# Optimization experiments

Hardware: AMD Instinct MI355X
Metric: run time of the kernel (lower is better)

The kernel has to match this reference:

```python
import jax, jax.numpy as jnp
import numpy as np

L, D, H, DK, DFF = 6, 768, 12, 64, 3072
VOCAB, NUM_BUCKETS, MAX_DIST = 32128, 32, 128
B, S = 8, 512
NEG = -1e9


def t5_layer_norm(x, w, eps=1e-6):
    var = jnp.mean(jnp.square(x), axis=-1, keepdims=True)
    return w * x * jax.lax.rsqrt(var + eps)


def relative_position_bucket(rel, num_buckets=NUM_BUCKETS, max_distance=MAX_DIST):
    # bidirectional T5 bucketing
    nb = num_buckets // 2
    ret = (rel > 0).astype(jnp.int32) * nb
    n = jnp.abs(rel)
    max_exact = nb // 2
    is_small = n < max_exact
    logf = jnp.log(jnp.maximum(n, 1).astype(jnp.float32) / max_exact)
    val_large = max_exact + (logf / np.log(max_distance / max_exact) * (nb - max_exact)).astype(jnp.int32)
    val_large = jnp.minimum(val_large, nb - 1)
    return ret + jnp.where(is_small, n, val_large)


def setup_inputs() -> dict:
    key = jax.random.key(0)
    ks = jax.random.split(key, 9)
    w = 0.02  # weight scale for numeric stability over 6 blocks
    return {
        "input_ids": jax.random.randint(ks[0], (B, S), 0, VOCAB),
        "attention_mask": jnp.ones((B, S), jnp.float32),
        "embed_w": jax.random.normal(ks[1], (VOCAB, D), jnp.float32),
        "ln1_w": jnp.ones((L, D), jnp.float32),
        "q_w": jax.random.normal(ks[2], (L, H * DK, D), jnp.float32) * w,
        "k_w": jax.random.normal(ks[3], (L, H * DK, D), jnp.float32) * w,
        "v_w": jax.random.normal(ks[4], (L, H * DK, D), jnp.float32) * w,
        "rel_bias_w": jax.random.normal(ks[5], (NUM_BUCKETS, H), jnp.float32),
        "o_w": jax.random.normal(ks[6], (L, D, H * DK), jnp.float32) * w,
        "ln2_w": jnp.ones((L, D), jnp.float32),
        "wi_w": jax.random.normal(ks[7], (L, DFF, D), jnp.float32) * w,
        "wo_w": jax.random.normal(ks[8], (L, D, DFF), jnp.float32) * w,
        "final_ln_w": jnp.ones((D,), jnp.float32),
    }


def reference(input_ids, attention_mask, embed_w, ln1_w, q_w, k_w, v_w,
              rel_bias_w, o_w, ln2_w, wi_w, wo_w, final_ln_w):
    b, s = input_ids.shape
    h = embed_w[input_ids]  # [B,S,D]

    # position bias computed once (block 0 owns the table; shared by all blocks)
    pos = jnp.arange(s)
    rel = pos[None, :] - pos[:, None]  # memory - query, [S,S]
    bucket = relative_position_bucket(rel)
    pos_bias = rel_bias_w[bucket]  # [S,S,H]
    pos_bias = jnp.transpose(pos_bias, (2, 0, 1))[None]  # [1,H,S,S]
    ext_mask = (1.0 - attention_mask)[:, None, None, :] * NEG  # [B,1,1,S]
    bias = pos_bias + ext_mask  # [B,H,S,S]

    for l in range(L):
        # --- self-attention (T5: no 1/sqrt(d) scaling) ---
        x = t5_layer_norm(h, ln1_w[l])
        q = jnp.einsum('bsd,id->bsi', x, q_w[l]).reshape(b, s, H, DK).transpose(0, 2, 1, 3)
        k = jnp.einsum('bsd,id->bsi', x, k_w[l]).reshape(b, s, H, DK).transpose(0, 2, 1, 3)
        v = jnp.einsum('bsd,id->bsi', x, v_w[l]).reshape(b, s, H, DK).transpose(0, 2, 1, 3)
        scores = jnp.einsum('bhqd,bhkd->bhqk', q, k) + bias
        attn = jax.nn.softmax(scores, axis=-1)
        ctx = jnp.einsum('bhqk,bhkd->bhqd', attn, v)
        ctx = ctx.transpose(0, 2, 1, 3).reshape(b, s, H * DK)
        h = h + jnp.einsum('bsi,di->bsd', ctx, o_w[l])
        # --- ReLU FFN ---
        x = t5_layer_norm(h, ln2_w[l])
        ff = jax.nn.relu(jnp.einsum('bsd,fd->bsf', x, wi_w[l]))
        h = h + jnp.einsum('bsf,df->bsd', ff, wo_w[l])

    return t5_layer_norm(h, final_ln_w)
```

## Files before the change

kernel.cpp:

```cpp
#include <hip/hip_runtime.h>
#include <hip/hip_bf16.h>
#include <math.h>

#define L_ 6
#define D_ 768
#define H_ 12
#define DK_ 64
#define DFF_ 3072
#define NB_ 32
#define MAXDIST_ 128
#define B_ 8
#define S_ 512
#define NEG_ (-1e9f)
#define BS_ (B_*S_)
#define BSD_ ((size_t)BS_*D_)
#define WLAYER_ 7077888

typedef __bf16 bf16x8 __attribute__((ext_vector_type(8)));
typedef float f32x4 __attribute__((ext_vector_type(4)));

__device__ __forceinline__ unsigned short f2bf(float f) {
    unsigned u = __float_as_uint(f);
    u += 0x7fff + ((u >> 16) & 1);
    return (unsigned short)(u >> 16);
}
__device__ __forceinline__ float bf2f(unsigned short s) {
    return __uint_as_float(((unsigned)s) << 16);
}

#define GLDS(g, l) __builtin_amdgcn_global_load_lds( \
    (const __attribute__((address_space(1))) void*)(const void*)(g), \
    (__attribute__((address_space(3))) void*)(void*)(l), 16, 0, 0)

__global__ __launch_bounds__(192) void k_embed(const int* __restrict__ ids,
                                               const float* __restrict__ ew,
                                               float* __restrict__ h) {
    int row = blockIdx.x;
    int id = ids[row];
    const float4* src = (const float4*)(ew + (size_t)id * D_);
    float4* dst = (float4*)(h + (size_t)row * D_);
    dst[threadIdx.x] = src[threadIdx.x];
}

template<int OUTBF>
__global__ __launch_bounds__(256) void k_rmsnorm(const float* __restrict__ in,
                                                 const float* __restrict__ w,
                                                 void* __restrict__ outp) {
    int row = blockIdx.x;
    int tid = threadIdx.x;
    const float* x = in + (size_t)row * D_;
    float ss = 0.f;
    for (int i = tid; i < D_; i += 256) { float v = x[i]; ss += v * v; }
    #pragma unroll
    for (int off = 32; off; off >>= 1) ss += __shfl_down(ss, off, 64);
    __shared__ float sbuf[4];
    if ((tid & 63) == 0) sbuf[tid >> 6] = ss;
    __syncthreads();
    float tot = sbuf[0] + sbuf[1] + sbuf[2] + sbuf[3];
    float scale = rsqrtf(tot / (float)D_ + 1e-6f);
    if (OUTBF) {
        unsigned short* o = (unsigned short*)outp + (size_t)row * D_;
        for (int i = tid; i < D_; i += 256) o[i] = f2bf(w[i] * x[i] * scale);
    } else {
        float* o = (float*)outp + (size_t)row * D_;
        for (int i = tid; i < D_; i += 256) o[i] = w[i] * x[i] * scale;
    }
}

__global__ __launch_bounds__(256) void k_posbias(const float* __restrict__ rbw,
                                                 unsigned short* __restrict__ biasg) {
    int idx = blockIdx.x * 256 + threadIdx.x;
    if (idx >= S_ * S_) return;
    int q = idx / S_, key = idx - q * S_;
    int rel = key - q;
    const int nb = NB_ / 2;
    int ret = rel > 0 ? nb : 0;
    int n = rel < 0 ? -rel : rel;
    const int max_exact = nb / 2;
    int val;
    if (n < max_exact) {
        val = n;
    } else {
        float lf = logf((float)n / (float)max_exact) /
                   logf((float)MAXDIST_ / (float)max_exact) * (float)(nb - max_exact);
        val = max_exact + (int)lf;
        if (val > nb - 1) val = nb - 1;
    }
    int bucket = ret + val;
    #pragma unroll
    for (int hh = 0; hh < H_; ++hh)
        biasg[((size_t)hh * S_ + q) * S_ + key] = f2bf(rbw[bucket * H_ + hh]);
}

#define W1V4 147456
#define W2V4 589824
#define WLV4 1769472
__global__ __launch_bounds__(256) void k_wconv_all(const float* __restrict__ qw,
                                                   const float* __restrict__ kw,
                                                   const float* __restrict__ vw,
                                                   const float* __restrict__ ow,
                                                   const float* __restrict__ wiw,
                                                   const float* __restrict__ wow,
                                                   unsigned short* __restrict__ wb) {
    int gid = blockIdx.x * 256 + threadIdx.x;
    int l = gid / WLV4;
    int i = gid - l * WLV4;
    const float* src;
    if (i < W1V4)                src = qw  + (size_t)l * 589824;
    else if ((i -= W1V4) < W1V4) src = kw  + (size_t)l * 589824;
    else if ((i -= W1V4) < W1V4) src = vw  + (size_t)l * 589824;
    else if ((i -= W1V4) < W1V4) src = ow  + (size_t)l * 589824;
    else if ((i -= W1V4) < W2V4) src = wiw + (size_t)l * 2359296;
    else { i -= W2V4;            src = wow + (size_t)l * 2359296; }
    float4 a = ((const float4*)src)[i];
    ushort4 o4;
    o4.x = f2bf(a.x); o4.y = f2bf(a.y); o4.z = f2bf(a.z); o4.w = f2bf(a.w);
    ((ushort4*)wb)[gid] = o4;
}

template<int BM, int BN>
__device__ __forceinline__ void stage_tile_t(const unsigned short* __restrict__ Abase,
                                             const unsigned short* __restrict__ Bbase,
                                             int k0, int K, int buf,
                                             unsigned short* lsA, unsigned short* lsB,
                                             int w, int lane) {
    constexpr int CA = BM / 32, CB = BN / 32;
    #pragma unroll
    for (int c = 0; c < CA; ++c) {
        int off = c * 4096 + w * 1024 + lane * 16;
        int row = off >> 7;
        int sc = (off & 127) ^ ((row & 7) << 4);
        GLDS(Abase + (size_t)row * K + k0 + (sc >> 1), (char*)lsA + buf * (BM * 128) + off);
    }
    #pragma unroll
    for (int c = 0; c < CB; ++c) {
        int off = c * 4096 + w * 1024 + lane * 16;
        int row = off >> 7;
        int sc = (off & 127) ^ ((row & 7) << 4);
        GLDS(Bbase + (size_t)row * K + k0 + (sc >> 1), (char*)lsB + buf * (BN * 128) + off);
    }
}

template<int BM, int BN>
__device__ __forceinline__ void gemm_compute_t(const char* cA, const char* cB,
                                               f32x4 acc[BM / 32][BN / 32],
                                               int l15, int l4, int wr, int wc) {
    constexpr int MI = BM / 32, NJ = BN / 32;
    #pragma unroll
    for (int kk = 0; kk < 2; ++kk) {
        bf16x8 af[MI], bfr[NJ];
        int kByte = kk * 64 + l4 * 16;
        #pragma unroll
        for (int i = 0; i < MI; ++i) {
            int r = wr + i * 16 + l15;
            af[i] = *(const bf16x8*)(cA + r * 128 + (kByte ^ ((r & 7) << 4)));
        }
        #pragma unroll
        for (int j = 0; j < NJ; ++j) {
            int r = wc + j * 16 + l15;
            bfr[j] = *(const bf16x8*)(cB + r * 128 + (kByte ^ ((r & 7) << 4)));
        }
        #pragma unroll
        for (int i = 0; i < MI; ++i)
            #pragma unroll
            for (int j = 0; j < NJ; ++j)
                acc[i][j] = __builtin_amdgcn_mfma_f32_16x16x32_bf16(af[i], bfr[j], acc[i][j], 0, 0, 0);
    }
}

template<int BM, int BN>
__device__ __forceinline__ void gemm_core_t(const unsigned short* __restrict__ A,
                                            const unsigned short* __restrict__ Bw,
                                            int K, int bm, int bn,
                                            unsigned short* lsA, unsigned short* lsB,
                                            f32x4 acc[BM / 32][BN / 32]) {
    int t = threadIdx.x, lane = t & 63, w = t >> 6;
    int l15 = lane & 15, l4 = lane >> 4;
    int wr = (w >> 1) * (BM / 2), wc = (w & 1) * (BN / 2);
    const unsigned short* Abase = A + (size_t)(bm * BM) * K;
    const unsigned short* Bbase = Bw + (size_t)(bn * BN) * K;
    int nt = K >> 6;
    constexpr int NL = BM / 32 + BN / 32;

    stage_tile_t<BM, BN>(Abase, Bbase, 0, K, 0, lsA, lsB, w, lane);
    for (int tq = 0; tq < nt - 1; ++tq) {
        int cur = tq & 1;
        stage_tile_t<BM, BN>(Abase, Bbase, (tq + 1) << 6, K, cur ^ 1, lsA, lsB, w, lane);
        if constexpr (NL == 8)      asm volatile("s_waitcnt vmcnt(8)" ::: "memory");
        else if constexpr (NL == 6) asm volatile("s_waitcnt vmcnt(6)" ::: "memory");
        else                        asm volatile("s_waitcnt vmcnt(4)" ::: "memory");
        __builtin_amdgcn_s_barrier();
        gemm_compute_t<BM, BN>((const char*)lsA + cur * (BM * 128),
                               (const char*)lsB + cur * (BN * 128), acc, l15, l4, wr, wc);
        asm volatile("s_waitcnt lgkmcnt(0)" ::: "memory");
        __builtin_amdgcn_s_barrier();
    }
    int cur = (nt - 1) & 1;
    asm volatile("s_waitcnt vmcnt(0)" ::: "memory");
    __builtin_amdgcn_s_barrier();
    gemm_compute_t<BM, BN>((const char*)lsA + cur * (BM * 128),
                           (const char*)lsB + cur * (BN * 128), acc, l15, l4, wr, wc);
}

template<int BM, int BN, int RES, int RELU, int OUTBF>
__global__ __launch_bounds__(256) void k_gemm_t(const unsigned short* __restrict__ A,
                                                const unsigned short* __restrict__ Bw,
                                                const float* __restrict__ res,
                                                void* __restrict__ C, int N, int K) {
    __shared__ __align__(16) unsigned short lsA[2 * BM * 64];
    __shared__ __align__(16) unsigned short lsB[2 * BN * 64];
    f32x4 acc[BM / 32][BN / 32] = {};
    int bm = blockIdx.x, bn = blockIdx.y;
    gemm_core_t<BM, BN>(A, Bw, K, bm, bn, lsA, lsB, acc);
    int t = threadIdx.x, lane = t & 63, w = t >> 6;
    int l15 = lane & 15, l4 = lane >> 4;
    int wr = (w >> 1) * (BM / 2), wc = (w & 1) * (BN / 2);
    #pragma unroll
    for (int i = 0; i < BM / 32; ++i) {
        #pragma unroll
        for (int r = 0; r < 4; ++r) {
            int row = bm * BM + wr + i * 16 + l4 * 4 + r;
            #pragma unroll
            for (int j = 0; j < BN / 32; ++j) {
                int col = bn * BN + wc + j * 16 + l15;
                float v = acc[i][j][r];
                if (RES)  v += res[(size_t)row * N + col];
                if (RELU) v = fmaxf(v, 0.f);
                if (OUTBF) ((unsigned short*)C)[(size_t)row * N + col] = f2bf(v);
                else       ((float*)C)[(size_t)row * N + col] = v;
            }
        }
    }
}

__global__ __launch_bounds__(256) void k_gemm_qkv_bf(const unsigned short* __restrict__ X,
                                                     const unsigned short* __restrict__ wq,
                                                     const unsigned short* __restrict__ wk,
                                                     const unsigned short* __restrict__ wv,
                                                     unsigned short* __restrict__ qo,
                                                     unsigned short* __restrict__ ko,
                                                     unsigned short* __restrict__ vt) {
    __shared__ __align__(16) unsigned short lsA[2 * 64 * 64];
    __shared__ __align__(16) unsigned short lsB[2 * 128 * 64];
    f32x4 acc[2][4] = {};
    int z = blockIdx.z;
    const unsigned short* Bm = z == 0 ? wq : (z == 1 ? wk : wv);
    int bm = blockIdx.x, bn = blockIdx.y;
    gemm_core_t<64, 128>(X, Bm, D_, bm, bn, lsA, lsB, acc);
    int t = threadIdx.x, lane = t & 63, w = t >> 6;
    int l15 = lane & 15, l4 = lane >> 4;
    int wr = (w >> 1) * 32, wc = (w & 1) * 64;
    if (z < 2) {
        unsigned short* C = z == 0 ? qo : ko;
        #pragma unroll
        for (int i = 0; i < 2; ++i)
            #pragma unroll
            for (int r = 0; r < 4; ++r) {
                int row = bm * 64 + wr + i * 16 + l4 * 4 + r;
                #pragma unroll
                for (int j = 0; j < 4; ++j) {
                    int col = bn * 128 + wc + j * 16 + l15;
                    C[(size_t)row * D_ + col] = f2bf(acc[i][j][r]);
                }
            }
    } else {
        #pragma unroll
        for (int i = 0; i < 2; ++i) {
            int row0 = bm * 64 + wr + i * 16 + l4 * 4;
            int b = row0 >> 9, s0 = row0 & 511;
            #pragma unroll
            for (int j = 0; j < 4; ++j) {
                int col = bn * 128 + wc + j * 16 + l15;
                int hh = col >> 6, dv = col & 63;
                ushort4 o4;
                o4.x = f2bf(acc[i][j][0]); o4.y = f2bf(acc[i][j][1]);
                o4.z = f2bf(acc[i][j][2]); o4.w = f2bf(acc[i][j][3]);
                *(ushort4*)(vt + (((size_t)b * H_ + hh) * 64 + dv) * S_ + s0) = o4;
            }
        }
    }
}

__global__ __launch_bounds__(256) void k_attn_flash(const unsigned short* __restrict__ qb,
                                                    const unsigned short* __restrict__ kb,
                                                    const unsigned short* __restrict__ vtb,
                                                    const unsigned short* __restrict__ biasg,
                                                    const float* __restrict__ mask,
                                                    unsigned short* __restrict__ ctx) {
    __shared__ __align__(16) unsigned short Kt[2][64 * 64];
    __shared__ __align__(16) unsigned short Vt[2][64 * 64];
    __shared__ __align__(16) unsigned short Pt[4][16 * 64];

    int t = threadIdx.x, lane = t & 63, w = t >> 6;
    int l15 = lane & 15, l4 = lane >> 4;
    int bh = blockIdx.y;
    int b = bh / H_, hh = bh - b * H_;
    int qblk = blockIdx.x;
    int qloc = w * 16 + l15;
    int qg = qblk * 64 + qloc;

    bf16x8 qf[2];
    {
        const unsigned short* qp = qb + ((size_t)(b * S_ + qg)) * D_ + hh * DK_;
        qf[0] = *(const bf16x8*)(qp + l4 * 8);
        qf[1] = *(const bf16x8*)(qp + 32 + l4 * 8);
    }
    float mrun = -1e30f, lsum = 0.f;
    f32x4 cacc[4] = {};

    auto stage_kv = [&](int kt, int buf) {
        int kbase = kt * 64;
        #pragma unroll
        for (int c = 0; c < 2; ++c) {
            int off = (w * 2 + c) * 1024 + lane * 16;
            int row = off >> 7;
            int colb = (off & 127) ^ ((row & 7) << 4);
            GLDS(kb + ((size_t)(b * S_ + kbase + row)) * D_ + hh * DK_ + (colb >> 1),
                 (char*)Kt[buf] + off);
            GLDS(vtb + ((size_t)bh * 64 + row) * S_ + kbase + (colb >> 1),
                 (char*)Vt[buf] + off);
        }
    };

    stage_kv(0, 0);
    const unsigned short* bprow = biasg + ((size_t)hh * S_ + qblk * 64 + qloc) * S_;

    for (int kt = 0; kt < S_ / 64; ++kt) {
        int cur = kt & 1;
        int kbase = kt * 64;
        ushort4 b4[4];
        float4 m4[4];
        #pragma unroll
        for (int j = 0; j < 4; ++j) {
            b4[j] = *(const ushort4*)(bprow + kbase + j * 16 + l4 * 4);
            m4[j] = *(const float4*)(mask + (size_t)b * S_ + kbase + j * 16 + l4 * 4);
        }
        if (kt < S_ / 64 - 1) {
            stage_kv(kt + 1, cur ^ 1);
            asm volatile("s_waitcnt vmcnt(4)" ::: "memory");
        } else {
            asm volatile("s_waitcnt vmcnt(0)" ::: "memory");
        }
        __builtin_amdgcn_s_barrier();

        f32x4 sc[4] = {};
        __builtin_amdgcn_s_setprio(1);
        #pragma unroll
        for (int kk = 0; kk < 2; ++kk) {
            int kByte = kk * 64 + l4 * 16;
            #pragma unroll
            for (int j = 0; j < 4; ++j) {
                int r = j * 16 + l15;
                bf16x8 kf = *(const bf16x8*)((const char*)Kt[cur] + r * 128 + (kByte ^ ((r & 7) << 4)));
                sc[j] = __builtin_amdgcn_mfma_f32_16x16x32_bf16(kf, qf[kk], sc[j], 0, 0, 0);
            }
        }
        __builtin_amdgcn_s_setprio(0);

        float sv[4][4];
        float tmax = -1e30f;
        #pragma unroll
        for (int j = 0; j < 4; ++j) {
            sv[j][0] = sc[j][0] + bf2f(b4[j].x) + (1.f - m4[j].x) * NEG_;
            sv[j][1] = sc[j][1] + bf2f(b4[j].y) + (1.f - m4[j].y) * NEG_;
            sv[j][2] = sc[j][2] + bf2f(b4[j].z) + (1.f - m4[j].z) * NEG_;
            sv[j][3] = sc[j][3] + bf2f(b4[j].w) + (1.f - m4[j].w) * NEG_;
            tmax = fmaxf(tmax, fmaxf(fmaxf(sv[j][0], sv[j][1]), fmaxf(sv[j][2], sv[j][3])));
        }
        tmax = fmaxf(tmax, __shfl_xor(tmax, 16, 64));
        tmax = fmaxf(tmax, __shfl_xor(tmax, 32, 64));
        float mnew = fmaxf(mrun, tmax);
        float scal = __expf(mrun - mnew);
        #pragma unroll
        for (int i = 0; i < 4; ++i) {
            cacc[i][0] *= scal; cacc[i][1] *= scal;
            cacc[i][2] *= scal; cacc[i][3] *= scal;
        }
        float psum = 0.f;
        unsigned pp[8];
        #pragma unroll
        for (int j = 0; j < 4; ++j) {
            float p0 = __expf(sv[j][0] - mnew), p1 = __expf(sv[j][1] - mnew);
            float p2 = __expf(sv[j][2] - mnew), p3 = __expf(sv[j][3] - mnew);
            psum += (p0 + p1) + (p2 + p3);
            pp[j * 2]     = (unsigned)f2bf(p0) | ((unsigned)f2bf(p1) << 16);
            pp[j * 2 + 1] = (unsigned)f2bf(p2) | ((unsigned)f2bf(p3) << 16);
        }
        lsum = lsum * scal + psum;
        mrun = mnew;
        unsigned short* P = Pt[w];
        #pragma unroll
        for (int j = 0; j < 4; ++j) {
            int base = l15 * 128 + ((j * 32 + l4 * 8) ^ ((l15 & 7) << 4));
            *(unsigned*)((char*)P + base) = pp[j * 2];
            *(unsigned*)((char*)P + base + 4) = pp[j * 2 + 1];
        }
        __builtin_amdgcn_s_setprio(1);
        #pragma unroll
        for (int kk = 0; kk < 2; ++kk) {
            int kByte = kk * 64 + l4 * 16;
            bf16x8 pf = *(const bf16x8*)((const char*)P + l15 * 128 + (kByte ^ ((l15 & 7) << 4)));
            #pragma unroll
            for (int i = 0; i < 4; ++i) {
                int rr = i * 16 + l15;
                bf16x8 vf = *(const bf16x8*)((const char*)Vt[cur] + rr * 128 + (kByte ^ ((rr & 7) << 4)));
                cacc[i] = __builtin_amdgcn_mfma_f32_16x16x32_bf16(vf, pf, cacc[i], 0, 0, 0);
            }
        }
        __builtin_amdgcn_s_setprio(0);
        asm volatile("s_waitcnt lgkmcnt(0)" ::: "memory");
        __builtin_amdgcn_s_barrier();
    }
    lsum += __shfl_xor(lsum, 16, 64);
    lsum += __shfl_xor(lsum, 32, 64);
    float inv = 1.f / lsum;
    unsigned short* cp = ctx + ((size_t)(b * S_ + qg)) * D_ + hh * DK_;
    #pragma unroll
    for (int i = 0; i < 4; ++i) {
        ushort4 o4;
        o4.x = f2bf(cacc[i][0] * inv); o4.y = f2bf(cacc[i][1] * inv);
        o4.z = f2bf(cacc[i][2] * inv); o4.w = f2bf(cacc[i][3] * inv);
        *(ushort4*)(cp + i * 16 + l4 * 4) = o4;
    }
}

extern "C" void kernel_launch(void* const* d_in, const int* in_sizes, int n_in,
                              void* d_out, int out_size, void* d_ws, size_t ws_size,
                              hipStream_t stream) {
    const int*   ids  = (const int*)d_in[0];
    const float* mask = (const float*)d_in[1];
    const float* ew   = (const float*)d_in[2];
    const float* ln1  = (const float*)d_in[3];
    const float* qw   = (const float*)d_in[4];
    const float* kw   = (const float*)d_in[5];
    const float* vw   = (const float*)d_in[6];
    const float* rbw  = (const float*)d_in[7];
    const float* ow   = (const float*)d_in[8];
    const float* ln2  = (const float*)d_in[9];
    const float* wiw  = (const float*)d_in[10];
    const float* wow  = (const float*)d_in[11];
    const float* flnw = (const float*)d_in[12];
    float* out = (float*)d_out;

    char* p = (char*)d_ws;
    float* h = (float*)p;                        p += BSD_ * 4;
    unsigned short* biasg = (unsigned short*)p;  p += (size_t)H_ * S_ * S_ * 2;
    unsigned short* wball = (unsigned short*)p;  p += (size_t)L_ * WLAYER_ * 2;
    unsigned short* xbf   = (unsigned short*)p;  p += BSD_ * 2;
    unsigned short* ctxb  = xbf;
    unsigned short* qbB   = (unsigned short*)p;  p += BSD_ * 2;
    unsigned short* kbB   = (unsigned short*)p;  p += BSD_ * 2;
    unsigned short* vtb   = (unsigned short*)p;  p += BSD_ * 2;
                    p += BSD_ * 2;
    unsigned short* ff    = qbB;

    k_embed<<<BS_, 192, 0, stream>>>(ids, ew, h);
    k_posbias<<<(S_ * S_ + 255) / 256, 256, 0, stream>>>(rbw, biasg);
    k_wconv_all<<<(L_ * WLV4) / 256, 256, 0, stream>>>(qw, kw, vw, ow, wiw, wow, wball);

    for (int l = 0; l < L_; ++l) {
        const unsigned short* wl  = wball + (size_t)l * WLAYER_;
        const unsigned short* wq  = wl;
        const unsigned short* wk  = wl + 589824;
        const unsigned short* wv  = wl + 1179648;
        const unsigned short* wo  = wl + 1769472;
        const unsigned short* wwi = wl + 2359296;
        const unsigned short* wwo = wl + 4718592;

        k_rmsnorm<1><<<BS_, 256, 0, stream>>>(h, ln1 + (size_t)l * D_, xbf);
        k_gemm_qkv_bf<<<dim3(BS_ / 64, D_ / 128, 3), 256, 0, stream>>>(
            xbf, wq, wk, wv, qbB, kbB, vtb);
        k_attn_flash<<<dim3(S_ / 64, B_ * H_), 256, 0, stream>>>(
            qbB, kbB, vtb, biasg, mask, ctxb);
        k_gemm_t<64, 64, 1, 0, 0><<<dim3(BS_ / 64, D_ / 64), 256, 0, stream>>>(
            ctxb, wo, h, h, D_, D_);
        k_rmsnorm<1><<<BS_, 256, 0, stream>>>(h, ln2 + (size_t)l * D_, xbf);
        k_gemm_t<64, 128, 0, 1, 1><<<dim3(BS_ / 64, DFF_ / 128), 256, 0, stream>>>(
            xbf, wwi, nullptr, ff, DFF_, D_);
        k_gemm_t<64, 64, 1, 0, 0><<<dim3(BS_ / 64, D_ / 64), 256, 0, stream>>>(
            ff, wwo, h, h, D_, DFF_);
    }
    k_rmsnorm<0><<<BS_, 256, 0, stream>>>(h, flnw, out);
}
```

Before: 892.7 us.

## Vectorize rmsnorm, batch weight conversion loads, prefetch attention bias and mask

The RMSNorm kernel now does one float4 load per thread and keeps the row in registers instead of reading it twice with scalar loads. The weight-conversion kernel handles four float4s per thread with loads issued ahead of stores, and launches a quarter as many blocks. The flash-attention kernel precomputes the extended mask once into shared memory and prefetches the next tile's position bias into registers one iteration ahead, so those global loads are off the critical path. In exchange the attention kernel uses more LDS and registers, which could lower occupancy.

After: 865.6 us. 1.03x faster.

```diff
diff --git a/kernel.cpp b/kernel.cpp
--- a/kernel.cpp
+++ b/kernel.cpp
@@ -48,9 +48,10 @@
                                                  void* __restrict__ outp) {
     int row = blockIdx.x;
     int tid = threadIdx.x;
-    const float* x = in + (size_t)row * D_;
-    float ss = 0.f;
-    for (int i = tid; i < D_; i += 256) { float v = x[i]; ss += v * v; }
+    const float4* x4 = (const float4*)(in + (size_t)row * D_);
+    float4 v = make_float4(0.f, 0.f, 0.f, 0.f);
+    if (tid < 192) v = x4[tid];
+    float ss = v.x * v.x + v.y * v.y + v.z * v.z + v.w * v.w;
     #pragma unroll
     for (int off = 32; off; off >>= 1) ss += __shfl_down(ss, off, 64);
     __shared__ float sbuf[4];
@@ -58,12 +59,17 @@
     __syncthreads();
     float tot = sbuf[0] + sbuf[1] + sbuf[2] + sbuf[3];
     float scale = rsqrtf(tot / (float)D_ + 1e-6f);
-    if (OUTBF) {
-        unsigned short* o = (unsigned short*)outp + (size_t)row * D_;
-        for (int i = tid; i < D_; i += 256) o[i] = f2bf(w[i] * x[i] * scale);
-    } else {
-        float* o = (float*)outp + (size_t)row * D_;
-        for (int i = tid; i < D_; i += 256) o[i] = w[i] * x[i] * scale;
+    if (tid < 192) {
+        float4 wv = ((const float4*)w)[tid];
+        float o0 = wv.x * v.x * scale, o1 = wv.y * v.y * scale;
+        float o2 = wv.z * v.z * scale, o3 = wv.w * v.w * scale;
+        if (OUTBF) {
+            ushort4 u;
+            u.x = f2bf(o0); u.y = f2bf(o1); u.z = f2bf(o2); u.w = f2bf(o3);
+            ((ushort4*)outp)[(size_t)row * 192 + tid] = u;
+        } else {
+            ((float4*)outp)[(size_t)row * 192 + tid] = make_float4(o0, o1, o2, o3);
+        }
     }
 }
 
@@ -102,20 +108,31 @@
                                                    const float* __restrict__ wiw,
                                                    const float* __restrict__ wow,
                                                    unsigned short* __restrict__ wb) {
-    int gid = blockIdx.x * 256 + threadIdx.x;
-    int l = gid / WLV4;
-    int i = gid - l * WLV4;
-    const float* src;
-    if (i < W1V4)                src = qw  + (size_t)l * 589824;
-    else if ((i -= W1V4) < W1V4) src = kw  + (size_t)l * 589824;
-    else if ((i -= W1V4) < W1V4) src = vw  + (size_t)l * 589824;
-    else if ((i -= W1V4) < W1V4) src = ow  + (size_t)l * 589824;
-    else if ((i -= W1V4) < W2V4) src = wiw + (size_t)l * 2359296;
-    else { i -= W2V4;            src = wow + (size_t)l * 2359296; }
-    float4 a = ((const float4*)src)[i];
-    ushort4 o4;
-    o4.x = f2bf(a.x); o4.y = f2bf(a.y); o4.z = f2bf(a.z); o4.w = f2bf(a.w);
-    ((ushort4*)wb)[gid] = o4;
+    int base = blockIdx.x * 1024 + threadIdx.x;
+    float4 a[4];
+    int gidv[4];
+    #pragma unroll
+    for (int k = 0; k < 4; ++k) {
+        int gid = base + k * 256;
+        gidv[k] = gid;
+        int l = gid / WLV4;
+        int i = gid - l * WLV4;
+        const float* src;
+        if (i < W1V4)                src = qw  + (size_t)l * 589824;
+        else if ((i -= W1V4) < W1V4) src = kw  + (size_t)l * 589824;
+        else if ((i -= W1V4) < W1V4) src = vw  + (size_t)l * 589824;
+        else if ((i -= W1V4) < W1V4) src = ow  + (size_t)l * 589824;
+        else if ((i -= W1V4) < W2V4) src = wiw + (size_t)l * 2359296;
+        else { i -= W2V4;            src = wow + (size_t)l * 2359296; }
+        a[k] = ((const float4*)src)[i];
+    }
+    #pragma unroll
+    for (int k = 0; k < 4; ++k) {
+        ushort4 o4;
+        o4.x = f2bf(a[k].x); o4.y = f2bf(a[k].y);
+        o4.z = f2bf(a[k].z); o4.w = f2bf(a[k].w);
+        ((ushort4*)wb)[gidv[k]] = o4;
+    }
 }
 
 template<int BM, int BN>
@@ -290,6 +307,7 @@
     __shared__ __align__(16) unsigned short Kt[2][64 * 64];
     __shared__ __align__(16) unsigned short Vt[2][64 * 64];
     __shared__ __align__(16) unsigned short Pt[4][16 * 64];
+    __shared__ __align__(16) float emask[S_];
 
     int t = threadIdx.x, lane = t & 63, w = t >> 6;
     int l15 = lane & 15, l4 = lane >> 4;
@@ -322,26 +340,43 @@
         }
     };
 
+    const unsigned short* bprow = biasg + ((size_t)hh * S_ + qblk * 64 + qloc) * S_;
+
     stage_kv(0, 0);
-    const unsigned short* bprow = biasg + ((size_t)hh * S_ + qblk * 64 + qloc) * S_;
-
-    for (int kt = 0; kt < S_ / 64; ++kt) {
+    if (t < 128) {
+        float4 m = ((const float4*)(mask + (size_t)b * S_))[t];
+        float4 e;
+        e.x = (1.f - m.x) * NEG_; e.y = (1.f - m.y) * NEG_;
+        e.z = (1.f - m.z) * NEG_; e.w = (1.f - m.w) * NEG_;
+        *(float4*)&emask[t * 4] = e;
+    }
+    ushort4 bnxt[4];
+    #pragma unroll
+    for (int j = 0; j < 4; ++j)
+        bnxt[j] = *(const ushort4*)(bprow + j * 16 + l4 * 4);
+    asm volatile("s_waitcnt lgkmcnt(0)" ::: "memory");
+    __builtin_amdgcn_s_barrier();
+
+    constexpr int NT = S_ / 64;
+    for (int kt = 0; kt < NT; ++kt) {
         int cur = kt & 1;
         int kbase = kt * 64;
-        ushort4 b4[4];
-        float4 m4[4];
-        #pragma unroll
-        for (int j = 0; j < 4; ++j) {
-            b4[j] = *(const ushort4*)(bprow + kbase + j * 16 + l4 * 4);
-            m4[j] = *(const float4*)(mask + (size_t)b * S_ + kbase + j * 16 + l4 * 4);
-        }
-        if (kt < S_ / 64 - 1) {
+        ushort4 bcur[4];
+        #pragma unroll
+        for (int j = 0; j < 4; ++j) bcur[j] = bnxt[j];
+
+        if (kt < NT - 1) {
             stage_kv(kt + 1, cur ^ 1);
             asm volatile("s_waitcnt vmcnt(4)" ::: "memory");
         } else {
             asm volatile("s_waitcnt vmcnt(0)" ::: "memory");
         }
         __builtin_amdgcn_s_barrier();
+        if (kt < NT - 1) {
+            #pragma unroll
+            for (int j = 0; j < 4; ++j)
+                bnxt[j] = *(const ushort4*)(bprow + (kt + 1) * 64 + j * 16 + l4 * 4);
+        }
 
         f32x4 sc[4] = {};
         __builtin_amdgcn_s_setprio(1);
@@ -361,10 +396,11 @@
         float tmax = -1e30f;
         #pragma unroll
         for (int j = 0; j < 4; ++j) {
-            sv[j][0] = sc[j][0] + bf2f(b4[j].x) + (1.f - m4[j].x) * NEG_;
-            sv[j][1] = sc[j][1] + bf2f(b4[j].y) + (1.f - m4[j].y) * NEG_;
-            sv[j][2] = sc[j][2] + bf2f(b4[j].z) + (1.f - m4[j].z) * NEG_;
-            sv[j][3] = sc[j][3] + bf2f(b4[j].w) + (1.f - m4[j].w) * NEG_;
+            float4 e4 = *(const float4*)&emask[kbase + j * 16 + l4 * 4];
+            sv[j][0] = sc[j][0] + bf2f(bcur[j].x) + e4.x;
+            sv[j][1] = sc[j][1] + bf2f(bcur[j].y) + e4.y;
+            sv[j][2] = sc[j][2] + bf2f(bcur[j].z) + e4.z;
+            sv[j][3] = sc[j][3] + bf2f(bcur[j].w) + e4.w;
             tmax = fmaxf(tmax, fmaxf(fmaxf(sv[j][0], sv[j][1]), fmaxf(sv[j][2], sv[j][3])));
         }
         tmax = fmaxf(tmax, __shfl_xor(tmax, 16, 64));
@@ -456,7 +492,7 @@
 
     k_embed<<<BS_, 192, 0, stream>>>(ids, ew, h);
     k_posbias<<<(S_ * S_ + 255) / 256, 256, 0, stream>>>(rbw, biasg);
-    k_wconv_all<<<(L_ * WLV4) / 256, 256, 0, stream>>>(qw, kw, vw, ow, wiw, wow, wball);
+    k_wconv_all<<<(L_ * WLV4) / 1024, 256, 0, stream>>>(qw, kw, vw, ow, wiw, wow, wball);
 
     for (int l = 0; l < L_; ++l) {
         const unsigned short* wl  = wball + (size_t)l * WLAYER_;
```
